# Kernel optimization log

Measured on AMD Instinct MI355X. Metric: run time of the kernel, lower is better.

## Reference

```python
import jax, jax.numpy as jnp
import numpy as np

N = 50000
E = 800000
IN_DIM = 128
HID = 64
HEADS = 4

def _gat_layer(h, src, dst, W, al, ar, Wres, activation):
    # h: [N, F_in]; W: [F_in, HEADS*HID]; al/ar: [HEADS, HID]
    n = h.shape[0]
    ft = (h @ W).reshape(n, HEADS, HID)                    # [N,H,D]
    el = (ft * al).sum(-1)                                  # [N,H]
    er = (ft * ar).sum(-1)                                  # [N,H]
    e = jax.nn.leaky_relu(el[src] + er[dst], 0.2)           # [E,H]
    m = jax.ops.segment_max(e, dst, num_segments=n)         # per-dst max for stable softmax
    ex = jnp.exp(e - m[dst])
    den = jax.ops.segment_sum(ex, dst, num_segments=n)
    alpha = ex / den[dst]                                   # edge softmax [E,H]
    out = jax.ops.segment_sum(alpha[:, :, None] * ft[src], dst, num_segments=n)  # [N,H,D]
    res = (h @ Wres).reshape(n, HEADS, HID) if Wres is not None else h.reshape(n, HEADS, HID)
    out = out + res
    return activation(out) if activation is not None else out


def setup_inputs() -> dict:
    key = jax.random.key(0)
    ks = jax.random.split(key, 16)
    def lin(k, fi, fo):
        return jax.random.normal(k, (fi, fo), jnp.float32) / np.sqrt(fi)
    HD = HEADS * HID
    inp = {
        "h": jax.random.normal(ks[0], (N, IN_DIM), jnp.float32),
        "src": jax.random.randint(ks[1], (E,), 0, N, jnp.int32),
        "dst": jax.random.randint(ks[2], (E,), 0, N, jnp.int32),
        "W1": lin(ks[3], IN_DIM, HD),
        "Wr1": lin(ks[4], IN_DIM, HD),
        "al1": jax.random.normal(ks[5], (HEADS, HID), jnp.float32) * 0.1,
        "ar1": jax.random.normal(ks[6], (HEADS, HID), jnp.float32) * 0.1,
        "W2": lin(ks[7], HD, HD),
        "al2": jax.random.normal(ks[8], (HEADS, HID), jnp.float32) * 0.1,
        "ar2": jax.random.normal(ks[9], (HEADS, HID), jnp.float32) * 0.1,
        "W3": lin(ks[10], HD, HD),
        "al3": jax.random.normal(ks[11], (HEADS, HID), jnp.float32) * 0.1,
        "ar3": jax.random.normal(ks[12], (HEADS, HID), jnp.float32) * 0.1,
        "Wm1": lin(ks[13], HID, HID),
        "bm1": jnp.zeros((HID,), jnp.float32),
        "Wm2": lin(ks[14], HID, 1),
        "bm2": jnp.zeros((1,), jnp.float32),
    }
    return inp


def reference(h, src, dst, W1, Wr1, al1, ar1, W2, al2, ar2, W3, al3, ar3, Wm1, bm1, Wm2, bm2):
    x = _gat_layer(h, src, dst, W1, al1, ar1, Wr1, jax.nn.relu)   # [N,H,D]
    x = x.reshape(x.shape[0], -1)                                  # [N,H*D]
    x = _gat_layer(x, src, dst, W2, al2, ar2, None, jax.nn.relu)  # identity residual (in==H*D)
    x = x.reshape(x.shape[0], -1)
    x = _gat_layer(x, src, dst, W3, al3, ar3, None, None)
    hf = x.mean(1)                                                 # [N,HID]
    diff = jnp.abs(hf[src] - hf[dst])                              # [E,HID]
    z = jax.nn.relu(diff @ Wm1 + bm1)
    score = jax.nn.sigmoid(z @ Wm2 + bm2).squeeze(-1)              # [E]
    return score
```

## Files before the change

kernel.cpp:

```cpp
#include <hip/hip_runtime.h>
#include <hip/hip_bf16.h>

typedef unsigned short u16;
typedef unsigned char u8;
typedef __attribute__((ext_vector_type(8))) short bf16x8;
typedef __attribute__((ext_vector_type(4))) float f32x4;
typedef __attribute__((ext_vector_type(2))) float f32x2;

__device__ __forceinline__ float bf2f(u16 u){
  union { unsigned int i; float f; } v; v.i = ((unsigned int)u) << 16; return v.f;
}
__device__ __forceinline__ u16 f2bf(float f){
  union { float f; unsigned int i; } v; v.f = f;
  unsigned int lsb = (v.i >> 16) & 1u;
  v.i += 0x7fffu + lsb;
  return (u16)(v.i >> 16);
}
__device__ __forceinline__ unsigned pkbf(float a, float b){
  __hip_bfloat162 h = __float22bfloat162_rn(make_float2(a, b));
  union { __hip_bfloat162 h2; unsigned u; } c; c.h2 = h; return c.u;
}
__device__ __forceinline__ u8 f2fp8(float f){
  int p = __builtin_amdgcn_cvt_pk_fp8_f32(f, f, 0, false);
  return (u8)(p & 0xFF);
}

__global__ void k_sniff(const u16* __restrict__ p, int* __restrict__ flag){
  __shared__ int s[256];
  int tid = threadIdx.x;
  u16 v = p[2 * tid];
  int e = (v >> 7) & 0xFF;
  s[tid] = (e >= 100 && e <= 135) ? 1 : 0;
  __syncthreads();
  for (int off = 128; off; off >>= 1){
    if (tid < off) s[tid] += s[tid + off];
    __syncthreads();
  }
  if (tid == 0) *flag = (s[0] < 180) ? 1 : 0;
}

struct PrepEnt { const void* s; void* d; void* d2; int n; int K; int mode; int bstart; };
struct Prep16 { PrepEnt e[16]; };
__global__ void k_prep(Prep16 tab, const u16* __restrict__ hsrc){
  __shared__ int s[256];
  __shared__ u16 tl[32][33];
  {
    int tid = threadIdx.x;
    u16 v = hsrc[2 * tid];
    int e = (v >> 7) & 0xFF;
    s[tid] = (e >= 100 && e <= 135) ? 1 : 0;
    __syncthreads();
    for (int off = 128; off; off >>= 1){
      if (tid < off) s[tid] += s[tid + off];
      __syncthreads();
    }
  }
  const int flag = (s[0] < 180) ? 1 : 0;
  __syncthreads();

  const int bx = blockIdx.x;
  int y = 0;
  #pragma unroll
  for (int i = 1; i < 16; ++i) if (bx >= tab.e[i].bstart) y = i;
  PrepEnt en = tab.e[y];
  const int nblk = ((y < 15) ? tab.e[y + 1].bstart : (int)gridDim.x) - en.bstart;
  const int lb = bx - en.bstart;
  const int T = nblk * 256;
  const int t0 = lb * 256 + threadIdx.x;

  if (en.mode == 1){
    u16* d = (u16*)en.d;
    for (int i = t0; i < en.n; i += T){
      u16 o[4];
      if (flag){
        float4 v = ((const float4*)en.s)[i];
        o[0] = f2bf(v.x); o[1] = f2bf(v.y); o[2] = f2bf(v.z); o[3] = f2bf(v.w);
      } else {
        uint2 v = ((const uint2*)en.s)[i];
        o[0] = (u16)v.x; o[1] = (u16)(v.x >> 16); o[2] = (u16)v.y; o[3] = (u16)(v.y >> 16);
      }
      uint2 w; w.x = o[0] | ((unsigned)o[1] << 16); w.y = o[2] | ((unsigned)o[3] << 16);
      ((uint2*)d)[i] = w;
    }
  } else if (en.mode == 0){
    u16* d = (u16*)en.d;
    for (int i = t0; i < en.n; i += T){
      if (flag) d[i] = f2bf(((const float*)en.s)[i]);
      else      d[i] = ((const u16*)en.s)[i];
    }
  } else if (en.mode == 2){
    u16* wt = (u16*)en.d;
    const int K = en.K;
    const int tk = lb >> 3, tc = lb & 7;
    const int tx = threadIdx.x & 31, ty = threadIdx.x >> 5;
    #pragma unroll
    for (int r = 0; r < 4; ++r){
      int row = tk * 32 + ty + r * 8, col = tc * 32 + tx;
      u16 b;
      if (flag) b = f2bf(((const float*)en.s)[row * 256 + col]);
      else      b = ((const u16*)en.s)[row * 256 + col];
      tl[ty + r * 8][tx] = b;
    }
    __syncthreads();
    #pragma unroll
    for (int r = 0; r < 4; ++r){
      int c = tc * 32 + ty + r * 8, k = tk * 32 + tx;
      wt[(size_t)c * K + k] = tl[tx][ty + r * 8];
    }
  }
}

__global__ void k_scan1(int4* __restrict__ cnt4, int* __restrict__ rowptr,
                        int* __restrict__ bsums, int N){
  __shared__ int s[256];
  int i = blockIdx.x * 256 + threadIdx.x;
  int4 c = make_int4(0, 0, 0, 0);
  if (i < N) c = cnt4[i];
  int v = c.x + c.y + c.z + c.w;
  if (i < N) cnt4[i] = make_int4(0, c.x, c.x + c.y, c.x + c.y + c.z);
  s[threadIdx.x] = v; __syncthreads();
  for (int off = 1; off < 256; off <<= 1){
    int x = 0;
    if (threadIdx.x >= off) x = s[threadIdx.x - off];
    __syncthreads();
    s[threadIdx.x] += x;
    __syncthreads();
  }
  if (i < N) rowptr[i + 1] = s[threadIdx.x];
  if (threadIdx.x == 255) bsums[blockIdx.x] = s[255];
}
__global__ void k_scan2(int* __restrict__ bsums, int nb){
  __shared__ int s[256];
  int t = threadIdx.x;
  int v = (t < nb) ? bsums[t] : 0;
  s[t] = v; __syncthreads();
  for (int off = 1; off < 256; off <<= 1){
    int x = 0;
    if (t >= off) x = s[t - off];
    __syncthreads();
    s[t] += x;
    __syncthreads();
  }
  if (t < nb) bsums[t] = s[t] - v;
}
__global__ void k_scan3(int* __restrict__ rowptr, const int* __restrict__ bsums, int N){
  int i = blockIdx.x * 256 + threadIdx.x;
  if (i < N){
    rowptr[i + 1] += bsums[blockIdx.x];
    if (i == 0) rowptr[0] = 0;
  }
}
__global__ void k_place(const int* __restrict__ src, const int* __restrict__ dst,
                        const int* __restrict__ slot, const int* __restrict__ rowptr,
                        const int* __restrict__ cur4, int4* __restrict__ csrp, int E){
  const int T = gridDim.x * 256;
  for (int i = blockIdx.x * 256 + threadIdx.x; i < E; i += T){
    int d = dst[i];
    int base = cur4[(d << 2) | (i & 3)];
    csrp[rowptr[d] + base + slot[i]] = make_int4(src[i], d, i, 0);
  }
}
__global__ void k_extract(const int4* __restrict__ csrp, int* __restrict__ csrs, int E){
  int i = blockIdx.x * 256 + threadIdx.x;
  if (i < E) csrs[i] = csrp[i].x;
}

#define GWAIT6() asm volatile("s_waitcnt vmcnt(6)" ::: "memory")
#define GWAIT0() asm volatile("s_waitcnt vmcnt(0)" ::: "memory")
#define GBAR()   do { __builtin_amdgcn_s_barrier(); __builtin_amdgcn_sched_barrier(0); } while (0)

__global__ __launch_bounds__(256, 5) void mfma_gemm_v7(
    const u16* __restrict__ X, const u16* __restrict__ WT, const u16* __restrict__ WTr,
    u8* __restrict__ FT8, u16* __restrict__ XA,
    const u16* __restrict__ al, const u16* __restrict__ ar,
    float* __restrict__ el4, float* __restrict__ er4, int N, int K,
    const int* __restrict__ edst, int* __restrict__ slotp, int* __restrict__ cur4,
    int Etot, int do_csr)
{
  extern __shared__ u16 Bs[];
  const int wv = threadIdx.x >> 6;
  const int lane = threadIdx.x & 63;
  const int m = lane & 15;
  const int q = lane >> 4;
  const int mh = m & 7;
  const int row0 = blockIdx.x * 64 + wv * 16;
  const int col0 = blockIdx.y * 128;
  const u16* W = (blockIdx.z == 0) ? WT : WTr;

  f32x4 acc[8];
  #pragma unroll
  for (int t = 0; t < 8; ++t) acc[t] = (f32x4){0.f, 0.f, 0.f, 0.f};
  const int rA = row0 + m;
  const bool vA = rA < N;
  const u16* apA = X + (size_t)rA * K + q * 8;

  auto stageC = [&](int c, int buf){
    u16* base = Bs + buf * 8192;
    const u16* Wk = W + c * 64;
    #pragma unroll
    for (int j = 0; j < 4; ++j){
      int cbase = (j * 4 + wv) * 64;
      int ci = cbase + lane;
      int col = ci >> 3, slot = ci & 7;
      int gslot = slot ^ (col & 7);
      const u16* srcp = Wk + (size_t)(col0 + col) * K + gslot * 8;
      __builtin_amdgcn_global_load_lds((const unsigned int*)srcp,
                                       (unsigned int*)(base + cbase * 8), 16, 0, 0);
    }
  };
  auto loadA = [&](int c, bf16x8* a){
    const int kb = c * 64;
    bf16x8 z = {};
    a[0] = z; a[1] = z;
    if (vA){ a[0] = *(const bf16x8*)(apA + kb); a[1] = *(const bf16x8*)(apA + kb + 32); }
  };
  auto compute = [&](const u16* __restrict__ Bb, const bf16x8* a){
    #pragma unroll
    for (int ks = 0; ks < 2; ++ks){
      const int sb = ks * 4 + q;
      #pragma unroll
      for (int t = 0; t < 8; ++t){
        const u16* bp = Bb + (size_t)(t * 16 + m) * 64 + (size_t)(sb ^ mh) * 8;
        bf16x8 b = *(const bf16x8*)bp;
        acc[t] = __builtin_amdgcn_mfma_f32_16x16x32_bf16(b, a[ks], acc[t], 0, 0, 0);
      }
    }
  };

  const int nc = K >> 6;
  bf16x8 a0[2], a1[2];
  stageC(0, 0);
  loadA(0, a0);
  for (int c = 0; c < nc; c += 2){
    if (c + 1 < nc){ stageC(c + 1, 1); loadA(c + 1, a1); GWAIT6(); }
    else           { GWAIT0(); }
    GBAR();
    compute(Bs, a0);
    GBAR();
    if (c + 1 < nc){
      if (c + 2 < nc){ stageC(c + 2, 0); loadA(c + 2, a0); GWAIT6(); }
      else           { GWAIT0(); }
      GBAR();
      compute(Bs + 8192, a1);
      GBAR();
    }
  }

  int ce0 = 0, ce1 = 0, cp0 = 0, cp1 = 0;
  bool cb0 = false, cb1 = false;
  if (do_csr){
    const int nbk = gridDim.x * 4;
    const int bid = ((blockIdx.z * 2 + blockIdx.y) * gridDim.x) + blockIdx.x;
    const int epb = (Etot + nbk - 1) / nbk;
    const int elo = bid * epb;
    const int ehi = min(elo + epb, Etot);
    ce0 = elo + (int)threadIdx.x;
    ce1 = ce0 + 256;
    cb0 = ce0 < ehi; cb1 = ce1 < ehi;
    int d0 = 0, d1 = 0;
    if (cb0) d0 = edst[ce0];
    if (cb1) d1 = edst[ce1];
    if (cb0) cp0 = atomicAdd(&cur4[(d0 << 2) | (ce0 & 3)], 1);
    if (cb1) cp1 = atomicAdd(&cur4[(d1 << 2) | (ce1 & 3)], 1);
    for (int e = elo + (int)threadIdx.x + 512; e < ehi; e += 256){
      int dd = edst[e];
      slotp[e] = atomicAdd(&cur4[(dd << 2) | (e & 3)], 1);
    }
  }

  if (blockIdx.z == 0){
    uint2 alp[8], arp[8];
    #pragma unroll
    for (int t = 0; t < 8; ++t){
      alp[t] = *(const uint2*)(al + col0 + t * 16 + q * 4);
      arp[t] = *(const uint2*)(ar + col0 + t * 16 + q * 4);
    }
    auto halv = [](uint2 p, int r) -> float {
      unsigned w = (r < 2) ? p.x : p.y;
      return bf2f((u16)((r & 1) ? (w >> 16) : (w & 0xffff)));
    };
    float pe[2] = {0.f, 0.f}, pr[2] = {0.f, 0.f};
    #pragma unroll
    for (int t = 0; t < 8; ++t)
      #pragma unroll
      for (int r = 0; r < 4; ++r){
        pe[t >> 2] += acc[t][r] * halv(alp[t], r);
        pr[t >> 2] += acc[t][r] * halv(arp[t], r);
      }
    pe[0] += __shfl_xor(pe[0], 16); pe[0] += __shfl_xor(pe[0], 32);
    pe[1] += __shfl_xor(pe[1], 16); pe[1] += __shfl_xor(pe[1], 32);
    pr[0] += __shfl_xor(pr[0], 16); pr[0] += __shfl_xor(pr[0], 32);
    pr[1] += __shfl_xor(pr[1], 16); pr[1] += __shfl_xor(pr[1], 32);
    if (q == 0 && vA){
      *(float2*)(el4 + (size_t)rA * 4 + blockIdx.y * 2) = make_float2(pe[0], pe[1]);
      *(float2*)(er4 + (size_t)rA * 4 + blockIdx.y * 2) = make_float2(pr[0], pr[1]);
    }
    if (vA){
      u8* op = FT8 + (size_t)rA * 256 + col0 + q * 4;
      #pragma unroll
      for (int t = 0; t < 8; ++t){
        int pw = __builtin_amdgcn_cvt_pk_fp8_f32(acc[t][0], acc[t][1], 0, false);
        pw = __builtin_amdgcn_cvt_pk_fp8_f32(acc[t][2], acc[t][3], pw, true);
        *(int*)(op + t * 16) = pw;
      }
    }
  } else {
    if (vA){
      u16* op = XA + (size_t)rA * 256 + col0 + q * 4;
      #pragma unroll
      for (int t = 0; t < 8; ++t){
        uint2 w;
        w.x = pkbf(acc[t][0], acc[t][1]);
        w.y = pkbf(acc[t][2], acc[t][3]);
        *(uint2*)(op + t * 16) = w;
      }
    }
  }

  if (do_csr){
    if (cb0) slotp[ce0] = cp0;
    if (cb1) slotp[ce1] = cp1;
  }
}

__global__ __launch_bounds__(256) void aggregate8(
    const u8* __restrict__ ft8, const float* __restrict__ el4, const float* __restrict__ er4,
    const int* __restrict__ rowptr, const int* __restrict__ csrs,
    const u16* __restrict__ residb, u16* __restrict__ outb,
    u16* __restrict__ hf, int do_hf, int N)
{
  __shared__ float sal[4][4][17][4];
  __shared__ int   sof[4][4][16];
  const int w = threadIdx.x >> 6, lane = threadIdx.x & 63;
  const int g = lane >> 4, t = lane & 15;
  const int hd = t >> 2;
  const int d = blockIdx.x * 16 + w * 4 + g;
  const bool vd = d < N;
  int beg = 0, deg = 0;
  if (vd){ beg = rowptr[d]; deg = rowptr[d + 1] - beg; }
  int mdeg = deg;
  mdeg = max(mdeg, __shfl_xor(mdeg, 16));
  mdeg = max(mdeg, __shfl_xor(mdeg, 32));
  float4 erd = make_float4(0.f, 0.f, 0.f, 0.f);
  if (vd) erd = ((const float4*)er4)[d];

  f32x2 acc2[8];
  #pragma unroll
  for (int i = 0; i < 8; ++i) acc2[i] = (f32x2){0.f, 0.f};
  float den[4] = {0.f, 0.f, 0.f, 0.f};

  for (int c0 = 0; c0 < mdeg; c0 += 16){
    const int rem = deg - c0;
    float t0 = 0.f, t1 = 0.f, t2 = 0.f, t3 = 0.f; int s = 0;
    if (t < rem){
      s = csrs[beg + c0 + t];
      float4 ql = ((const float4*)el4)[s];
      float e0 = ql.x + erd.x; e0 = (e0 > 0.f) ? e0 : 0.2f * e0;
      float e1 = ql.y + erd.y; e1 = (e1 > 0.f) ? e1 : 0.2f * e1;
      float e2 = ql.z + erd.z; e2 = (e2 > 0.f) ? e2 : 0.2f * e2;
      float e3 = ql.w + erd.w; e3 = (e3 > 0.f) ? e3 : 0.2f * e3;
      t0 = __expf(fminf(e0, 60.f)); t1 = __expf(fminf(e1, 60.f));
      t2 = __expf(fminf(e2, 60.f)); t3 = __expf(fminf(e3, 60.f));
    }
    den[0] += t0; den[1] += t1; den[2] += t2; den[3] += t3;
    sal[w][g][t][0] = t0; sal[w][g][t][1] = t1;
    sal[w][g][t][2] = t2; sal[w][g][t][3] = t3;
    sof[w][g][t] = s << 8;
    __builtin_amdgcn_wave_barrier();
    int cr = rem < 16 ? (rem < 0 ? 0 : rem) : 16;
    int jm = (cr + 3) & ~3;
    for (int j = 0; j < jm; j += 4){
      float a[4]; unsigned off[4]; uint4 v[4];
      #pragma unroll
      for (int u = 0; u < 4; ++u){
        a[u] = sal[w][g][j + u][hd];
        off[u] = (unsigned)sof[w][g][j + u];
      }
      #pragma unroll
      for (int u = 0; u < 4; ++u)
        v[u] = *(const uint4*)(ft8 + (size_t)off[u] + t * 16);
      #pragma unroll
      for (int u = 0; u < 4; ++u){
        f32x2 a2 = (f32x2){a[u], a[u]};
        acc2[0] += __builtin_amdgcn_cvt_pk_f32_fp8(v[u].x, 0) * a2;
        acc2[1] += __builtin_amdgcn_cvt_pk_f32_fp8(v[u].x, 1) * a2;
        acc2[2] += __builtin_amdgcn_cvt_pk_f32_fp8(v[u].y, 0) * a2;
        acc2[3] += __builtin_amdgcn_cvt_pk_f32_fp8(v[u].y, 1) * a2;
        acc2[4] += __builtin_amdgcn_cvt_pk_f32_fp8(v[u].z, 0) * a2;
        acc2[5] += __builtin_amdgcn_cvt_pk_f32_fp8(v[u].z, 1) * a2;
        acc2[6] += __builtin_amdgcn_cvt_pk_f32_fp8(v[u].w, 0) * a2;
        acc2[7] += __builtin_amdgcn_cvt_pk_f32_fp8(v[u].w, 1) * a2;
      }
    }
    __builtin_amdgcn_wave_barrier();
  }
  #pragma unroll
  for (int mk = 1; mk < 16; mk <<= 1){
    den[0] += __shfl_xor(den[0], mk); den[1] += __shfl_xor(den[1], mk);
    den[2] += __shfl_xor(den[2], mk); den[3] += __shfl_xor(den[3], mk);
  }
  const float dh = den[hd];
  const float inv = (dh > 0.f) ? (1.f / dh) : 0.f;

  if (!vd) return;
  const u16* rp = residb + (size_t)d * 256 + t * 16;
  uint4 r0 = *(const uint4*)rp;
  uint4 r1 = *(const uint4*)(rp + 8);
  float o[16];
  {
    union { unsigned u; float f; } x;
    unsigned rw[8] = {r0.x, r0.y, r0.z, r0.w, r1.x, r1.y, r1.z, r1.w};
    #pragma unroll
    for (int i = 0; i < 8; ++i){
      x.u = rw[i] << 16;          o[2 * i]     = x.f;
      x.u = rw[i] & 0xffff0000u;  o[2 * i + 1] = x.f;
    }
  }
  #pragma unroll
  for (int i = 0; i < 8; ++i){
    o[2 * i]     += acc2[i].x * inv;
    o[2 * i + 1] += acc2[i].y * inv;
  }
  if (!do_hf){
    uint4 a, b;
    a.x = pkbf(fmaxf(o[0], 0.f),  fmaxf(o[1], 0.f));
    a.y = pkbf(fmaxf(o[2], 0.f),  fmaxf(o[3], 0.f));
    a.z = pkbf(fmaxf(o[4], 0.f),  fmaxf(o[5], 0.f));
    a.w = pkbf(fmaxf(o[6], 0.f),  fmaxf(o[7], 0.f));
    b.x = pkbf(fmaxf(o[8], 0.f),  fmaxf(o[9], 0.f));
    b.y = pkbf(fmaxf(o[10], 0.f), fmaxf(o[11], 0.f));
    b.z = pkbf(fmaxf(o[12], 0.f), fmaxf(o[13], 0.f));
    b.w = pkbf(fmaxf(o[14], 0.f), fmaxf(o[15], 0.f));
    u16* op = outb + (size_t)d * 256 + t * 16;
    *(uint4*)op = a;
    *(uint4*)(op + 8) = b;
  } else {
    #pragma unroll
    for (int i = 0; i < 16; ++i){
      float v = o[i];
      v += __shfl_xor(v, 4);
      v += __shfl_xor(v, 8);
      o[i] = 0.25f * v;
    }
    if (t < 4){
      uint4 a, b;
      a.x = pkbf(o[0], o[1]);   a.y = pkbf(o[2], o[3]);
      a.z = pkbf(o[4], o[5]);   a.w = pkbf(o[6], o[7]);
      b.x = pkbf(o[8], o[9]);   b.y = pkbf(o[10], o[11]);
      b.z = pkbf(o[12], o[13]); b.w = pkbf(o[14], o[15]);
      u16* hp = hf + (size_t)d * 64 + t * 16;
      *(uint4*)hp = a;
      *(uint4*)(hp + 8) = b;
    }
  }
}

__global__ __launch_bounds__(256) void edge_mlp_csr(
    const u16* __restrict__ hfb, const int4* __restrict__ csrp,
    const u16* __restrict__ Wm1, const u16* __restrict__ bm1,
    const u16* __restrict__ Wm2, const u16* __restrict__ bm2,
    void* __restrict__ out, int E, const int* __restrict__ flag)
{
  const int lane = threadIdx.x & 63;
  const int m = lane & 15;
  const int q = lane >> 4;
  const int is_f32 = *flag;

  bf16x8 bfr[4][2];
  #pragma unroll
  for (int t = 0; t < 4; ++t)
    #pragma unroll
    for (int ks = 0; ks < 2; ++ks)
      #pragma unroll
      for (int j = 0; j < 8; ++j)
        bfr[t][ks][j] = (short)Wm1[(size_t)(ks * 32 + q * 8 + j) * 64 + t * 16 + m];

  float b1v[4], w2v[4];
  #pragma unroll
  for (int t = 0; t < 4; ++t){
    b1v[t] = bf2f(bm1[t * 16 + m]);
    w2v[t] = bf2f(Wm2[t * 16 + m]);
  }
  const float b2 = bf2f(bm2[0]);

  const int wid = blockIdx.x * 4 + (threadIdx.x >> 6);
  const int nw  = gridDim.x * 4;
  for (int e0 = wid * 16; e0 < E; e0 += nw * 16){
    int e = e0 + m; if (e >= E) e = E - 1;
    int4 ed = csrp[e];
    const u16* ps = hfb + (size_t)ed.x * 64;
    const u16* pd = hfb + (size_t)ed.y * 64;
    union { bf16x8 v; uint4 u; } af[2];
    #pragma unroll
    for (int ks = 0; ks < 2; ++ks){
      bf16x8 vs = *(const bf16x8*)(ps + ks * 32 + q * 8);
      bf16x8 vd = *(const bf16x8*)(pd + ks * 32 + q * 8);
      unsigned pk[4];
      #pragma unroll
      for (int pp = 0; pp < 4; ++pp){
        float a0 = fabsf(bf2f((u16)vs[2 * pp])     - bf2f((u16)vd[2 * pp]));
        float a1 = fabsf(bf2f((u16)vs[2 * pp + 1]) - bf2f((u16)vd[2 * pp + 1]));
        pk[pp] = pkbf(a0, a1);
      }
      af[ks].u = make_uint4(pk[0], pk[1], pk[2], pk[3]);
    }
    f32x4 acc[4];
    #pragma unroll
    for (int t = 0; t < 4; ++t) acc[t] = (f32x4){0.f, 0.f, 0.f, 0.f};
    #pragma unroll
    for (int ks = 0; ks < 2; ++ks)
      #pragma unroll
      for (int t = 0; t < 4; ++t)
        acc[t] = __builtin_amdgcn_mfma_f32_16x16x32_bf16(af[ks].v, bfr[t][ks], acc[t], 0, 0, 0);
    #pragma unroll
    for (int r = 0; r < 4; ++r){
      float p = 0.f;
      #pragma unroll
      for (int t = 0; t < 4; ++t)
        p += fmaxf(acc[t][r] + b1v[t], 0.f) * w2v[t];
      #pragma unroll
      for (int mm = 1; mm < 16; mm <<= 1) p += __shfl_xor(p, mm);
      int slot = e0 + q * 4 + r;
      if (m == 0 && slot < E){
        int eid = csrp[slot].z;
        float sc = 1.f / (1.f + __expf(-(p + b2)));
        if (is_f32) ((float*)out)[eid] = sc;
        else        ((u16*)out)[eid]   = f2bf(sc);
      }
    }
  }
}

extern "C" void kernel_launch(void* const* d_in, const int* in_sizes, int n_in,
                              void* d_out, int out_size, void* d_ws, size_t ws_size,
                              hipStream_t stream)
{
  const int* src = (const int*)d_in[1];
  const int* dst = (const int*)d_in[2];

  const int N = in_sizes[0] / 128;
  const int E = in_sizes[1];

  char* p = (char*)d_ws;
  auto alloc = [&](size_t bytes) -> char* {
    char* r = p; p += (bytes + 255) & ~(size_t)255; return r;
  };
  int* flag   = (int*)  alloc(4);
  u16* hc     = (u16*)  alloc((size_t)N * 128 * 2);
  u8*  FT8    = (u8*)   alloc((size_t)N * 256);
  u16* XA     = (u16*)  alloc((size_t)N * 256 * 2);
  u16* XB     = (u16*)  alloc((size_t)N * 256 * 2);
  float* el   = (float*)alloc((size_t)N * 4 * 4);
  float* er   = (float*)alloc((size_t)N * 4 * 4);
  u16* hfb    = (u16*)  alloc((size_t)N * 64 * 2);
  int* rowptr = (int*)  alloc((size_t)(N + 1) * 4);
  int* cur4   = (int*)  alloc((size_t)N * 16);
  int* slot   = (int*)  alloc((size_t)E * 4);
  int4* csrp  = (int4*) alloc((size_t)E * 16);
  int* csrs   = (int*)  alloc((size_t)E * 4);
  int* bsums  = (int*)  alloc(1024);
  u16* WT1    = (u16*)  alloc(128 * 256 * 2);
  u16* WTr1   = (u16*)  alloc(128 * 256 * 2);
  u16* WT2    = (u16*)  alloc(256 * 256 * 2);
  u16* WT3    = (u16*)  alloc(256 * 256 * 2);
  u16* al1c   = (u16*)  alloc(256 * 2);
  u16* ar1c   = (u16*)  alloc(256 * 2);
  u16* al2c   = (u16*)  alloc(256 * 2);
  u16* ar2c   = (u16*)  alloc(256 * 2);
  u16* al3c   = (u16*)  alloc(256 * 2);
  u16* ar3c   = (u16*)  alloc(256 * 2);
  u16* Wm1c   = (u16*)  alloc(4096 * 2);
  u16* bm1c   = (u16*)  alloc(64 * 2);
  u16* Wm2c   = (u16*)  alloc(64 * 2);
  u16* bm2c   = (u16*)  alloc(2);

  const int nb = (N + 255) / 256;
  const int ge = (E + 255) / 256;
  const u16* hsrc = (const u16*)d_in[0];

  k_sniff<<<1, 256, 0, stream>>>(hsrc, flag);
  hipMemsetAsync(cur4, 0, (size_t)N * 16, stream);

  {
    Prep16 t{};
    int b = 0;
    auto put = [&](int idx, const void* s, void* d, void* d2, int n, int K,
                   int mode, int nblk){
      t.e[idx] = {s, d, d2, n, K, mode, b};
      b += nblk;
    };
    put(0,  d_in[0],  hc,    nullptr, N * 32,   0,   1, 768);
    put(1,  d_in[3],  WT1,   nullptr, 0,        128, 2, 32);
    put(2,  d_in[4],  WTr1,  nullptr, 0,        128, 2, 32);
    put(3,  d_in[7],  WT2,   nullptr, 0,        256, 2, 64);
    put(4,  d_in[10], WT3,   nullptr, 0,        256, 2, 64);
    put(5,  d_in[5],  al1c,  nullptr, 256,      0,   0, 1);
    put(6,  d_in[6],  ar1c,  nullptr, 256,      0,   0, 1);
    put(7,  d_in[8],  al2c,  nullptr, 256,      0,   0, 1);
    put(8,  d_in[9],  ar2c,  nullptr, 256,      0,   0, 1);
    put(9,  d_in[11], al3c,  nullptr, 256,      0,   0, 1);
    put(10, d_in[12], ar3c,  nullptr, 256,      0,   0, 1);
    put(11, d_in[13], Wm1c,  nullptr, 4096,     0,   0, 1);
    put(12, d_in[14], bm1c,  nullptr, 64,       0,   0, 1);
    put(13, d_in[15], Wm2c,  nullptr, 64,       0,   0, 1);
    put(14, d_in[16], bm2c,  nullptr, 1,        0,   0, 1);
    put(15, nullptr,  nullptr, nullptr, 0,      0,   0, 0);
    k_prep<<<dim3(b), 256, 0, stream>>>(t, hsrc);
  }

  const dim3 gA3((N + 63) / 64, 2);
  const dim3 gL1((N + 63) / 64, 2, 2);
  const int gG = (N + 15) / 16;
  const int ldsP = 2 * 128 * 64 * 2;

  mfma_gemm_v7<<<gL1, 256, ldsP, stream>>>(hc, WT1, WTr1, FT8, XA, al1c, ar1c,
                                           el, er, N, 128, dst, slot, cur4, E, 1);
  k_scan1<<<nb, 256, 0, stream>>>((int4*)cur4, rowptr, bsums, N);
  k_scan2<<<1, 256, 0, stream>>>(bsums, nb);
  k_scan3<<<nb, 256, 0, stream>>>(rowptr, bsums, N);
  k_place<<<512, 256, 0, stream>>>(src, dst, slot, rowptr, cur4, csrp, E);
  k_extract<<<ge, 256, 0, stream>>>(csrp, csrs, E);

  aggregate8<<<gG, 256, 0, stream>>>(FT8, el, er, rowptr, csrs, XA, XB, nullptr, 0, N);
  mfma_gemm_v7<<<gA3, 256, ldsP, stream>>>(XB, WT2, WT2, FT8, XA, al2c, ar2c,
                                           el, er, N, 256, nullptr, nullptr, nullptr, 0, 0);
  aggregate8<<<gG, 256, 0, stream>>>(FT8, el, er, rowptr, csrs, XB, XA, nullptr, 0, N);
  mfma_gemm_v7<<<gA3, 256, ldsP, stream>>>(XA, WT3, WT3, FT8, XB, al3c, ar3c,
                                           el, er, N, 256, nullptr, nullptr, nullptr, 0, 0);
  aggregate8<<<gG, 256, 0, stream>>>(FT8, el, er, rowptr, csrs, XA, nullptr, hfb, 1, N);
  edge_mlp_csr<<<2048, 256, 0, stream>>>(hfb, csrp, Wm1c, bm1c, Wm2c, bm2c,
                                         d_out, E, flag);
}
```

Measured before the change: 394.9 us.

## Build CSR slots with per-block LDS histograms instead of global atomics in the GEMM

Adds a standalone kernel that builds the CSR slot positions. Each block owns a range of destination nodes, scans the whole dst array, and counts its nodes with LDS atomics. This removes the global-atomic counting that was fused into the first GEMM epilogue, the 4-way split counter array, and its memset, which simplifies the scan and place kernels. The cost is that every block rereads all of dst, so about 64 blocks each stream the full edge array, and the CSR build now runs before the GEMM instead of overlapping with it.

```diff
diff --git a/kernel.cpp b/kernel.cpp
--- a/kernel.cpp
+++ b/kernel.cpp
@@ -37,6 +37,35 @@
     __syncthreads();
   }
   if (tid == 0) *flag = (s[0] < 180) ? 1 : 0;
+}
+
+__global__ __launch_bounds__(1024) void k_csrpos(const int* __restrict__ dst,
+                                                 int* __restrict__ slot,
+                                                 int* __restrict__ cnt, int N, int E){
+  __shared__ int bins[1024];
+  const int nblk = gridDim.x;
+  const int R = (N + nblk - 1) / nblk;
+  const int lo = blockIdx.x * R;
+  const int hi = min(lo + R, N);
+  const int nb = hi - lo;
+  for (int i = threadIdx.x; i < nb; i += 1024) bins[i] = 0;
+  __syncthreads();
+  const int E4 = E >> 2;
+  for (int i = threadIdx.x; i < E4; i += 1024){
+    int4 d4 = ((const int4*)dst)[i];
+    int e = i << 2;
+    int x;
+    x = d4.x - lo; if ((unsigned)x < (unsigned)nb) slot[e]     = atomicAdd(&bins[x], 1);
+    x = d4.y - lo; if ((unsigned)x < (unsigned)nb) slot[e + 1] = atomicAdd(&bins[x], 1);
+    x = d4.z - lo; if ((unsigned)x < (unsigned)nb) slot[e + 2] = atomicAdd(&bins[x], 1);
+    x = d4.w - lo; if ((unsigned)x < (unsigned)nb) slot[e + 3] = atomicAdd(&bins[x], 1);
+  }
+  for (int e = (E4 << 2) + threadIdx.x; e < E; e += 1024){
+    int x = dst[e] - lo;
+    if ((unsigned)x < (unsigned)nb) slot[e] = atomicAdd(&bins[x], 1);
+  }
+  __syncthreads();
+  for (int i = threadIdx.x; i < nb; i += 1024) cnt[lo + i] = bins[i];
 }
 
 struct PrepEnt { const void* s; void* d; void* d2; int n; int K; int mode; int bstart; };
@@ -110,14 +139,11 @@
   }
 }
 
-__global__ void k_scan1(int4* __restrict__ cnt4, int* __restrict__ rowptr,
+__global__ void k_scan1(const int* __restrict__ cnt, int* __restrict__ rowptr,
                         int* __restrict__ bsums, int N){
   __shared__ int s[256];
   int i = blockIdx.x * 256 + threadIdx.x;
-  int4 c = make_int4(0, 0, 0, 0);
-  if (i < N) c = cnt4[i];
-  int v = c.x + c.y + c.z + c.w;
-  if (i < N) cnt4[i] = make_int4(0, c.x, c.x + c.y, c.x + c.y + c.z);
+  int v = (i < N) ? cnt[i] : 0;
   s[threadIdx.x] = v; __syncthreads();
   for (int off = 1; off < 256; off <<= 1){
     int x = 0;
@@ -152,12 +178,11 @@
 }
 __global__ void k_place(const int* __restrict__ src, const int* __restrict__ dst,
                         const int* __restrict__ slot, const int* __restrict__ rowptr,
-                        const int* __restrict__ cur4, int4* __restrict__ csrp, int E){
+                        int4* __restrict__ csrp, int E){
   const int T = gridDim.x * 256;
   for (int i = blockIdx.x * 256 + threadIdx.x; i < E; i += T){
     int d = dst[i];
-    int base = cur4[(d << 2) | (i & 3)];
-    csrp[rowptr[d] + base + slot[i]] = make_int4(src[i], d, i, 0);
+    csrp[rowptr[d] + slot[i]] = make_int4(src[i], d, i, 0);
   }
 }
 __global__ void k_extract(const int4* __restrict__ csrp, int* __restrict__ csrs, int E){
@@ -173,9 +198,7 @@
     const u16* __restrict__ X, const u16* __restrict__ WT, const u16* __restrict__ WTr,
     u8* __restrict__ FT8, u16* __restrict__ XA,
     const u16* __restrict__ al, const u16* __restrict__ ar,
-    float* __restrict__ el4, float* __restrict__ er4, int N, int K,
-    const int* __restrict__ edst, int* __restrict__ slotp, int* __restrict__ cur4,
-    int Etot, int do_csr)
+    float* __restrict__ el4, float* __restrict__ er4, int N, int K)
 {
   extern __shared__ u16 Bs[];
   const int wv = threadIdx.x >> 6;
@@ -246,28 +269,6 @@
     }
   }
 
-  int ce0 = 0, ce1 = 0, cp0 = 0, cp1 = 0;
-  bool cb0 = false, cb1 = false;
-  if (do_csr){
-    const int nbk = gridDim.x * 4;
-    const int bid = ((blockIdx.z * 2 + blockIdx.y) * gridDim.x) + blockIdx.x;
-    const int epb = (Etot + nbk - 1) / nbk;
-    const int elo = bid * epb;
-    const int ehi = min(elo + epb, Etot);
-    ce0 = elo + (int)threadIdx.x;
-    ce1 = ce0 + 256;
-    cb0 = ce0 < ehi; cb1 = ce1 < ehi;
-    int d0 = 0, d1 = 0;
-    if (cb0) d0 = edst[ce0];
-    if (cb1) d1 = edst[ce1];
-    if (cb0) cp0 = atomicAdd(&cur4[(d0 << 2) | (ce0 & 3)], 1);
-    if (cb1) cp1 = atomicAdd(&cur4[(d1 << 2) | (ce1 & 3)], 1);
-    for (int e = elo + (int)threadIdx.x + 512; e < ehi; e += 256){
-      int dd = edst[e];
-      slotp[e] = atomicAdd(&cur4[(dd << 2) | (e & 3)], 1);
-    }
-  }
-
   if (blockIdx.z == 0){
     uint2 alp[8], arp[8];
     #pragma unroll
@@ -315,11 +316,6 @@
         *(uint2*)(op + t * 16) = w;
       }
     }
-  }
-
-  if (do_csr){
-    if (cb0) slotp[ce0] = cp0;
-    if (cb1) slotp[ce1] = cp1;
   }
 }
 
@@ -554,7 +550,7 @@
   float* er   = (float*)alloc((size_t)N * 4 * 4);
   u16* hfb    = (u16*)  alloc((size_t)N * 64 * 2);
   int* rowptr = (int*)  alloc((size_t)(N + 1) * 4);
-  int* cur4   = (int*)  alloc((size_t)N * 16);
+  int* cnt    = (int*)  alloc((size_t)N * 4);
   int* slot   = (int*)  alloc((size_t)E * 4);
   int4* csrp  = (int4*) alloc((size_t)E * 16);
   int* csrs   = (int*)  alloc((size_t)E * 4);
@@ -579,7 +575,12 @@
   const u16* hsrc = (const u16*)d_in[0];
 
   k_sniff<<<1, 256, 0, stream>>>(hsrc, flag);
-  hipMemsetAsync(cur4, 0, (size_t)N * 16, stream);
+
+  {
+    int nbp = (N + 1023) / 1024;
+    if (nbp < 64) nbp = 64;
+    k_csrpos<<<nbp, 1024, 0, stream>>>(dst, slot, cnt, N, E);
+  }
 
   {
     Prep16 t{};
@@ -608,25 +609,25 @@
     k_prep<<<dim3(b), 256, 0, stream>>>(t, hsrc);
   }
 
+  k_scan1<<<nb, 256, 0, stream>>>(cnt, rowptr, bsums, N);
+  k_scan2<<<1, 256, 0, stream>>>(bsums, nb);
+  k_scan3<<<nb, 256, 0, stream>>>(rowptr, bsums, N);
+  k_place<<<512, 256, 0, stream>>>(src, dst, slot, rowptr, csrp, E);
+  k_extract<<<ge, 256, 0, stream>>>(csrp, csrs, E);
+
   const dim3 gA3((N + 63) / 64, 2);
   const dim3 gL1((N + 63) / 64, 2, 2);
   const int gG = (N + 15) / 16;
   const int ldsP = 2 * 128 * 64 * 2;
 
   mfma_gemm_v7<<<gL1, 256, ldsP, stream>>>(hc, WT1, WTr1, FT8, XA, al1c, ar1c,
-                                           el, er, N, 128, dst, slot, cur4, E, 1);
-  k_scan1<<<nb, 256, 0, stream>>>((int4*)cur4, rowptr, bsums, N);
-  k_scan2<<<1, 256, 0, stream>>>(bsums, nb);
-  k_scan3<<<nb, 256, 0, stream>>>(rowptr, bsums, N);
-  k_place<<<512, 256, 0, stream>>>(src, dst, slot, rowptr, cur4, csrp, E);
-  k_extract<<<ge, 256, 0, stream>>>(csrp, csrs, E);
-
+                                           el, er, N, 128);
   aggregate8<<<gG, 256, 0, stream>>>(FT8, el, er, rowptr, csrs, XA, XB, nullptr, 0, N);
   mfma_gemm_v7<<<gA3, 256, ldsP, stream>>>(XB, WT2, WT2, FT8, XA, al2c, ar2c,
-                                           el, er, N, 256, nullptr, nullptr, nullptr, 0, 0);
+                                           el, er, N, 256);
   aggregate8<<<gG, 256, 0, stream>>>(FT8, el, er, rowptr, csrs, XB, XA, nullptr, 0, N);
   mfma_gemm_v7<<<gA3, 256, ldsP, stream>>>(XA, WT3, WT3, FT8, XB, al3c, ar3c,
-                                           el, er, N, 256, nullptr, nullptr, nullptr, 0, 0);
+                                           el, er, N, 256);
   aggregate8<<<gG, 256, 0, stream>>>(FT8, el, er, rowptr, csrs, XA, nullptr, hfb, 1, N);
   edge_mlp_csr<<<2048, 256, 0, stream>>>(hfb, csrp, Wm1c, bm1c, Wm2c, bm2c,
                                          d_out, E, flag);
```

Result: slower. 459.7 us (+16.4%).
